# Performance work log

Hardware: AMD Instinct MI355X
Metric: run time of the kernel (lower is better)

Reference implementation:

```python
import jax, jax.numpy as jnp
import numpy as np

N = 100000   # nodes
E = 1000000  # edges per block
P = 100000   # pos/neg link edges
IN = 128
H = 64


def setup_inputs() -> dict:
    key = jax.random.key(0)
    ks = jax.random.split(key, 24)
    d = {}
    d["x"] = jax.random.normal(ks[0], (N, IN), jnp.float32)
    d["edge_weight"] = jax.random.uniform(ks[1], (3, E), jnp.float32)
    d["src"] = jax.random.randint(ks[2], (E,), 0, N)
    d["dst"] = jax.random.randint(ks[3], (E,), 0, N)
    d["pos_src"] = jax.random.randint(ks[4], (P,), 0, N)
    d["pos_dst"] = jax.random.randint(ks[5], (P,), 0, N)
    d["neg_src"] = jax.random.randint(ks[6], (P,), 0, N)
    d["neg_dst"] = jax.random.randint(ks[7], (P,), 0, N)
    s = 1.0 / np.sqrt(IN)
    h = 1.0 / np.sqrt(H)
    d["W0"] = jax.random.normal(ks[8], (IN, H), jnp.float32) * s
    d["b0"] = jnp.zeros((H,), jnp.float32)
    d["W1"] = jax.random.normal(ks[9], (H, H), jnp.float32) * h
    d["b1"] = jnp.zeros((H,), jnp.float32)
    d["W2"] = jax.random.normal(ks[10], (H, H), jnp.float32) * h
    d["b2"] = jnp.zeros((H,), jnp.float32)
    d["P0"] = jax.random.normal(ks[11], (H, H), jnp.float32) * h
    d["pb0"] = jnp.zeros((H,), jnp.float32)
    d["P1"] = jax.random.normal(ks[12], (H, H), jnp.float32) * h
    d["pb1"] = jnp.zeros((H,), jnp.float32)
    d["P2"] = jax.random.normal(ks[13], (H, 1), jnp.float32) * h
    d["pb2"] = jnp.zeros((1,), jnp.float32)
    return d


def _graph_conv(h, W, b, src, dst, ew, n_nodes):
    # DGL GraphConv, norm='both': D_out^{-1/2} on source feats,
    # edge-weighted sum aggregation, D_in^{-1/2} on result, then linear.
    ones = jnp.ones(src.shape[0], h.dtype)
    deg_out = jax.ops.segment_sum(ones, src, num_segments=n_nodes)
    deg_in = jax.ops.segment_sum(ones, dst, num_segments=n_nodes)
    norm_src = jax.lax.rsqrt(jnp.maximum(deg_out, 1.0))
    norm_dst = jax.lax.rsqrt(jnp.maximum(deg_in, 1.0))
    # apply weight before aggregation (in_feats >= out_feats); math-equivalent either way
    hw = (h * norm_src[:, None]) @ W            # [N, H]
    msg = hw[src] * ew[:, None]                 # [E, H] gather + scale
    agg = jax.ops.segment_sum(msg, dst, num_segments=n_nodes)  # scatter-add
    return agg * norm_dst[:, None] + b


def reference(x, edge_weight, src, dst, pos_src, pos_dst, neg_src, neg_dst,
              W0, b0, W1, b1, W2, b2, P0, pb0, P1, pb1, P2, pb2):
    h = jax.nn.relu(_graph_conv(x, W0, b0, src, dst, edge_weight[0], N))
    h = jax.nn.relu(_graph_conv(h, W1, b1, src, dst, edge_weight[1], N))
    h = _graph_conv(h, W2, b2, src, dst, edge_weight[2], N)  # no relu on last layer

    def mlp(z):
        z = jax.nn.relu(z @ P0 + pb0)
        z = jax.nn.relu(z @ P1 + pb1)
        return z @ P2 + pb2

    h_pos = mlp(h[pos_src] * h[pos_dst])  # [P, 1]
    h_neg = mlp(h[neg_src] * h[neg_dst])  # [P, 1]
    return (h_pos, h_neg)
```

## Files before the change

kernel.cpp:

```cpp
#include <hip/hip_runtime.h>


#define NN 100000
#define NE 1000000
#define NP 100000
#define SCAN_NB 98

__device__ __forceinline__ void row_fma(float4& acc, float xv, const float4& wv) {
    acc.x = fmaf(xv, wv.x, acc.x);
    acc.y = fmaf(xv, wv.y, acc.y);
    acc.z = fmaf(xv, wv.z, acc.z);
    acc.w = fmaf(xv, wv.w, acc.w);
}

__global__ void deg_kernel(const int4* __restrict__ src4, const int4* __restrict__ dst4,
                           int* __restrict__ repl, int E4) {
    int xcc;
    asm volatile("s_getreg_b32 %0, hwreg(HW_REG_XCC_ID)" : "=s"(xcc));
    xcc &= 7;
    int* dout = repl + xcc * NN;
    int* din  = repl + (8 + xcc) * NN;
    int tid = blockIdx.x * blockDim.x + threadIdx.x;
    if (tid < E4) {
        int4 s = src4[tid], d = dst4[tid];
        __hip_atomic_fetch_add(&dout[s.x], 1, __ATOMIC_RELAXED, __HIP_MEMORY_SCOPE_WORKGROUP);
        __hip_atomic_fetch_add(&dout[s.y], 1, __ATOMIC_RELAXED, __HIP_MEMORY_SCOPE_WORKGROUP);
        __hip_atomic_fetch_add(&dout[s.z], 1, __ATOMIC_RELAXED, __HIP_MEMORY_SCOPE_WORKGROUP);
        __hip_atomic_fetch_add(&dout[s.w], 1, __ATOMIC_RELAXED, __HIP_MEMORY_SCOPE_WORKGROUP);
        __hip_atomic_fetch_add(&din[d.x], 1, __ATOMIC_RELAXED, __HIP_MEMORY_SCOPE_WORKGROUP);
        __hip_atomic_fetch_add(&din[d.y], 1, __ATOMIC_RELAXED, __HIP_MEMORY_SCOPE_WORKGROUP);
        __hip_atomic_fetch_add(&din[d.z], 1, __ATOMIC_RELAXED, __HIP_MEMORY_SCOPE_WORKGROUP);
        __hip_atomic_fetch_add(&din[d.w], 1, __ATOMIC_RELAXED, __HIP_MEMORY_SCOPE_WORKGROUP);
    }
}

__global__ void reduce_norm_kernel(const int* __restrict__ repl, float* __restrict__ norm_src,
                                   float* __restrict__ norm_dst, int* __restrict__ deg_in, int n) {
    int i = blockIdx.x * blockDim.x + threadIdx.x;
    if (i < n) {
        int so = 0, si = 0;
#pragma unroll
        for (int x = 0; x < 8; ++x) {
            so += repl[x * NN + i];
            si += repl[(8 + x) * NN + i];
        }
        norm_src[i] = rsqrtf(fmaxf((float)so, 1.0f));
        norm_dst[i] = rsqrtf(fmaxf((float)si, 1.0f));
        deg_in[i] = si;
    }
}

__global__ __launch_bounds__(1024) void scan_block(const int* __restrict__ deg,
                                                   int* __restrict__ tmp_excl,
                                                   int* __restrict__ blocksums, int n) {
    __shared__ int wsums[16];
    const int i = blockIdx.x * 1024 + threadIdx.x;
    const int lane = threadIdx.x & 63, w = threadIdx.x >> 6;
    int v = (i < n) ? deg[i] : 0;
    int s = v;
#pragma unroll
    for (int off = 1; off < 64; off <<= 1) {
        int u = __shfl_up(s, off, 64);
        if (lane >= off) s += u;
    }
    if (lane == 63) wsums[w] = s;
    __syncthreads();
    if (w == 0) {
        int wv = (lane < 16) ? wsums[lane] : 0;
#pragma unroll
        for (int off = 1; off < 16; off <<= 1) {
            int u = __shfl_up(wv, off, 64);
            if (lane >= off) wv += u;
        }
        if (lane < 16) wsums[lane] = wv;
    }
    __syncthreads();
    int excl = s - v + (w > 0 ? wsums[w - 1] : 0);
    if (i < n) tmp_excl[i] = excl;
    if (threadIdx.x == 1023) blocksums[blockIdx.x] = excl + v;
}

__global__ void scan_sums(int* __restrict__ bs, int nb) {
    __shared__ int wtot[2];
    const int t = threadIdx.x;
    const int lane = t & 63, w = t >> 6;
    int v = (t < nb) ? bs[t] : 0;
    int s = v;
#pragma unroll
    for (int off = 1; off < 64; off <<= 1) {
        int u = __shfl_up(s, off, 64);
        if (lane >= off) s += u;
    }
    if (lane == 63) wtot[w] = s;
    __syncthreads();
    int excl = s - v + (w == 1 ? wtot[0] : 0);
    if (t < nb) bs[t] = excl;
}

__global__ __launch_bounds__(1024) void scan_apply(const int* __restrict__ tmp_excl,
                                                   const int* __restrict__ bs,
                                                   int* __restrict__ row_ptr,
                                                   int* __restrict__ cursor, int n) {
    const int i = blockIdx.x * 1024 + threadIdx.x;
    if (i < n) {
        int r = tmp_excl[i] + bs[blockIdx.x];
        row_ptr[i] = r;
        cursor[i] = r;
    }
    if (i == 0) row_ptr[n] = NE;
}

__global__ void csr_fill(const int* __restrict__ src, const int* __restrict__ dst,
                         const float* __restrict__ ew, int* __restrict__ cursor,
                         float4* __restrict__ cedge, int E) {
    int tid = blockIdx.x * blockDim.x + threadIdx.x;
    int stride = gridDim.x * blockDim.x;
    for (int e = tid; e < E; e += stride) {
        int d = dst[e];
        int slot = atomicAdd(&cursor[d], 1);
        float4 c;
        c.x = __int_as_float(src[e]);
        c.y = ew[e];
        c.z = ew[NE + e];
        c.w = ew[2 * NE + e];
        cedge[slot] = c;
    }
}

template <int WSEL, bool FINAL>
__global__ __launch_bounds__(256) void aggregate(const float* __restrict__ hw,
                                                 const float4* __restrict__ cedge,
                                                 const int* __restrict__ row_ptr,
                                                 const float* __restrict__ norm_src,
                                                 const float* __restrict__ norm_dst,
                                                 const float* __restrict__ bias,
                                                 float* __restrict__ outx, int n) {
    const int lane = threadIdx.x & 63;
    const int gw = (blockIdx.x * blockDim.x + threadIdx.x) >> 6;
    const int nw = (gridDim.x * blockDim.x) >> 6;
    const float blane = bias[lane];
    for (int node = gw; node < n; node += nw) {
        int beg = row_ptr[node], end = row_ptr[node + 1];
        float a0 = 0.f, a1 = 0.f, a2 = 0.f, a3 = 0.f;
        int i = beg;
        for (; i + 7 < end; i += 8) {
            float4 c0 = cedge[i + 0], c1 = cedge[i + 1], c2 = cedge[i + 2], c3 = cedge[i + 3];
            float4 c4 = cedge[i + 4], c5 = cedge[i + 5], c6 = cedge[i + 6], c7 = cedge[i + 7];
            float h0 = hw[__float_as_int(c0.x) * 64 + lane];
            float h1 = hw[__float_as_int(c1.x) * 64 + lane];
            float h2 = hw[__float_as_int(c2.x) * 64 + lane];
            float h3 = hw[__float_as_int(c3.x) * 64 + lane];
            float h4 = hw[__float_as_int(c4.x) * 64 + lane];
            float h5 = hw[__float_as_int(c5.x) * 64 + lane];
            float h6 = hw[__float_as_int(c6.x) * 64 + lane];
            float h7 = hw[__float_as_int(c7.x) * 64 + lane];
            a0 = fmaf(h0, (WSEL == 0) ? c0.y : (WSEL == 1) ? c0.z : c0.w, a0);
            a1 = fmaf(h1, (WSEL == 0) ? c1.y : (WSEL == 1) ? c1.z : c1.w, a1);
            a2 = fmaf(h2, (WSEL == 0) ? c2.y : (WSEL == 1) ? c2.z : c2.w, a2);
            a3 = fmaf(h3, (WSEL == 0) ? c3.y : (WSEL == 1) ? c3.z : c3.w, a3);
            a0 = fmaf(h4, (WSEL == 0) ? c4.y : (WSEL == 1) ? c4.z : c4.w, a0);
            a1 = fmaf(h5, (WSEL == 0) ? c5.y : (WSEL == 1) ? c5.z : c5.w, a1);
            a2 = fmaf(h6, (WSEL == 0) ? c6.y : (WSEL == 1) ? c6.z : c6.w, a2);
            a3 = fmaf(h7, (WSEL == 0) ? c7.y : (WSEL == 1) ? c7.z : c7.w, a3);
        }
        for (; i + 1 < end; i += 2) {
            float4 c0 = cedge[i], c1 = cedge[i + 1];
            float h0 = hw[__float_as_int(c0.x) * 64 + lane];
            float h1 = hw[__float_as_int(c1.x) * 64 + lane];
            a0 = fmaf(h0, (WSEL == 0) ? c0.y : (WSEL == 1) ? c0.z : c0.w, a0);
            a1 = fmaf(h1, (WSEL == 0) ? c1.y : (WSEL == 1) ? c1.z : c1.w, a1);
        }
        if (i < end) {
            float4 c0 = cedge[i];
            float h0 = hw[__float_as_int(c0.x) * 64 + lane];
            a0 = fmaf(h0, (WSEL == 0) ? c0.y : (WSEL == 1) ? c0.z : c0.w, a0);
        }
        float a = (a0 + a1) + (a2 + a3);
        float nd = norm_dst[node];
        float t;
        if (FINAL) {
            t = fmaf(a, nd, blane);
        } else {
            t = fmaxf(fmaf(a, nd, blane), 0.f) * norm_src[node];
        }
        outx[node * 64 + lane] = t;
    }
}

template <int K, bool SCALE>
__global__ __launch_bounds__(256, 5) void gemm_tile(const float* __restrict__ in,
                                                    const float* __restrict__ W,
                                                    const float* __restrict__ norm_src,
                                                    float* __restrict__ out, int n) {
    __shared__ float Ws[K * 64];
    const int tid = threadIdx.x;
    for (int i = tid; i < K * 16; i += 256) ((float4*)Ws)[i] = ((const float4*)W)[i];
    __syncthreads();

    const int tr = tid >> 4, tc = tid & 15;
    const int row0 = blockIdx.x * 64 + tr * 4;
    const float* xr0 = in + (size_t)min(row0 + 0, n - 1) * K;
    const float* xr1 = in + (size_t)min(row0 + 1, n - 1) * K;
    const float* xr2 = in + (size_t)min(row0 + 2, n - 1) * K;
    const float* xr3 = in + (size_t)min(row0 + 3, n - 1) * K;

    float4 acc0 = {0, 0, 0, 0}, acc1 = {0, 0, 0, 0}, acc2 = {0, 0, 0, 0}, acc3 = {0, 0, 0, 0};
#pragma unroll 4
    for (int k4 = 0; k4 < K / 4; ++k4) {
        const int kb = k4 * 4;
        float4 xv0 = *(const float4*)&xr0[kb];
        float4 xv1 = *(const float4*)&xr1[kb];
        float4 xv2 = *(const float4*)&xr2[kb];
        float4 xv3 = *(const float4*)&xr3[kb];
        const float* wb = &Ws[kb * 64 + tc * 4];
        float4 wk;
        wk = *(const float4*)(wb);
        row_fma(acc0, xv0.x, wk); row_fma(acc1, xv1.x, wk); row_fma(acc2, xv2.x, wk); row_fma(acc3, xv3.x, wk);
        wk = *(const float4*)(wb + 64);
        row_fma(acc0, xv0.y, wk); row_fma(acc1, xv1.y, wk); row_fma(acc2, xv2.y, wk); row_fma(acc3, xv3.y, wk);
        wk = *(const float4*)(wb + 128);
        row_fma(acc0, xv0.z, wk); row_fma(acc1, xv1.z, wk); row_fma(acc2, xv2.z, wk); row_fma(acc3, xv3.z, wk);
        wk = *(const float4*)(wb + 192);
        row_fma(acc0, xv0.w, wk); row_fma(acc1, xv1.w, wk); row_fma(acc2, xv2.w, wk); row_fma(acc3, xv3.w, wk);
    }

#pragma unroll
    for (int i = 0; i < 4; ++i) {
        int row = row0 + i;
        if (row < n) {
            float4 o = (i == 0) ? acc0 : (i == 1) ? acc1 : (i == 2) ? acc2 : acc3;
            if (SCALE) {
                float ns = norm_src[row];
                o.x *= ns; o.y *= ns; o.z *= ns; o.w *= ns;
            }
            *(float4*)&out[row * 64 + tc * 4] = o;
        }
    }
}

#define ZST 76

__global__ __launch_bounds__(256) void mlp_tile(const float* __restrict__ hfin,
                                                const float* __restrict__ P0,
                                                const float* __restrict__ pb0,
                                                const float* __restrict__ P1,
                                                const float* __restrict__ pb1,
                                                const float* __restrict__ P2,
                                                const float* __restrict__ pb2,
                                                const int* __restrict__ pos_src,
                                                const int* __restrict__ pos_dst,
                                                const int* __restrict__ neg_src,
                                                const int* __restrict__ neg_dst,
                                                float* __restrict__ out, int P) {
    __shared__ float Zs[64][ZST];
    __shared__ float pb0s[64], pb1s[64], P2s[64];
    __shared__ int pas[64], pbs[64];
    const int tid = threadIdx.x;
    const int base = blockIdx.x << 6;
    if (tid < 64) {
        pb0s[tid] = pb0[tid];
        pb1s[tid] = pb1[tid];
        P2s[tid] = P2[tid];
        int p = base + tid;
        pas[tid] = (p < P) ? pos_src[p] : neg_src[p - P];
        pbs[tid] = (p < P) ? pos_dst[p] : neg_dst[p - P];
    }
    const float pb2v = pb2[0];
    const int lane = tid & 63, w = tid >> 6;
    const int tr = tid >> 4, tc = tid & 15;
    __syncthreads();

    {
        const int pbase = w * 16;
#pragma unroll
        for (int r = 0; r < 2; ++r) {
            const int p0 = pbase + r * 8;
            int a0 = pas[p0 + 0], b0 = pbs[p0 + 0];
            int a1 = pas[p0 + 1], b1 = pbs[p0 + 1];
            int a2 = pas[p0 + 2], b2 = pbs[p0 + 2];
            int a3 = pas[p0 + 3], b3 = pbs[p0 + 3];
            int a4 = pas[p0 + 4], b4 = pbs[p0 + 4];
            int a5 = pas[p0 + 5], b5 = pbs[p0 + 5];
            int a6 = pas[p0 + 6], b6 = pbs[p0 + 6];
            int a7 = pas[p0 + 7], b7 = pbs[p0 + 7];
            float ha0 = hfin[a0 * 64 + lane], hb0 = hfin[b0 * 64 + lane];
            float ha1 = hfin[a1 * 64 + lane], hb1 = hfin[b1 * 64 + lane];
            float ha2 = hfin[a2 * 64 + lane], hb2 = hfin[b2 * 64 + lane];
            float ha3 = hfin[a3 * 64 + lane], hb3 = hfin[b3 * 64 + lane];
            float ha4 = hfin[a4 * 64 + lane], hb4 = hfin[b4 * 64 + lane];
            float ha5 = hfin[a5 * 64 + lane], hb5 = hfin[b5 * 64 + lane];
            float ha6 = hfin[a6 * 64 + lane], hb6 = hfin[b6 * 64 + lane];
            float ha7 = hfin[a7 * 64 + lane], hb7 = hfin[b7 * 64 + lane];
            Zs[p0 + 0][lane] = ha0 * hb0;
            Zs[p0 + 1][lane] = ha1 * hb1;
            Zs[p0 + 2][lane] = ha2 * hb2;
            Zs[p0 + 3][lane] = ha3 * hb3;
            Zs[p0 + 4][lane] = ha4 * hb4;
            Zs[p0 + 5][lane] = ha5 * hb5;
            Zs[p0 + 6][lane] = ha6 * hb6;
            Zs[p0 + 7][lane] = ha7 * hb7;
        }
    }
    __syncthreads();

    float4 acc0, acc1, acc2, acc3;
    {
        float4 binit = *(const float4*)&pb0s[tc * 4];
        acc0 = binit; acc1 = binit; acc2 = binit; acc3 = binit;
    }
#pragma unroll 4
    for (int k4 = 0; k4 < 16; ++k4) {
        const int kb = k4 * 4;
        float4 xv0 = *(const float4*)&Zs[tr * 4 + 0][kb];
        float4 xv1 = *(const float4*)&Zs[tr * 4 + 1][kb];
        float4 xv2 = *(const float4*)&Zs[tr * 4 + 2][kb];
        float4 xv3 = *(const float4*)&Zs[tr * 4 + 3][kb];
        const float* wb = &P0[kb * 64 + tc * 4];
        float4 wk;
        wk = *(const float4*)(wb);
        row_fma(acc0, xv0.x, wk); row_fma(acc1, xv1.x, wk); row_fma(acc2, xv2.x, wk); row_fma(acc3, xv3.x, wk);
        wk = *(const float4*)(wb + 64);
        row_fma(acc0, xv0.y, wk); row_fma(acc1, xv1.y, wk); row_fma(acc2, xv2.y, wk); row_fma(acc3, xv3.y, wk);
        wk = *(const float4*)(wb + 128);
        row_fma(acc0, xv0.z, wk); row_fma(acc1, xv1.z, wk); row_fma(acc2, xv2.z, wk); row_fma(acc3, xv3.z, wk);
        wk = *(const float4*)(wb + 192);
        row_fma(acc0, xv0.w, wk); row_fma(acc1, xv1.w, wk); row_fma(acc2, xv2.w, wk); row_fma(acc3, xv3.w, wk);
    }
    __syncthreads();
#pragma unroll
    for (int i = 0; i < 4; ++i) {
        float4 o = (i == 0) ? acc0 : (i == 1) ? acc1 : (i == 2) ? acc2 : acc3;
        o.x = fmaxf(o.x, 0.f); o.y = fmaxf(o.y, 0.f); o.z = fmaxf(o.z, 0.f); o.w = fmaxf(o.w, 0.f);
        *(float4*)&Zs[tr * 4 + i][tc * 4] = o;
    }
    __syncthreads();

    {
        float4 binit = *(const float4*)&pb1s[tc * 4];
        acc0 = binit; acc1 = binit; acc2 = binit; acc3 = binit;
    }
#pragma unroll 4
    for (int k4 = 0; k4 < 16; ++k4) {
        const int kb = k4 * 4;
        float4 xv0 = *(const float4*)&Zs[tr * 4 + 0][kb];
        float4 xv1 = *(const float4*)&Zs[tr * 4 + 1][kb];
        float4 xv2 = *(const float4*)&Zs[tr * 4 + 2][kb];
        float4 xv3 = *(const float4*)&Zs[tr * 4 + 3][kb];
        const float* wb = &P1[kb * 64 + tc * 4];
        float4 wk;
        wk = *(const float4*)(wb);
        row_fma(acc0, xv0.x, wk); row_fma(acc1, xv1.x, wk); row_fma(acc2, xv2.x, wk); row_fma(acc3, xv3.x, wk);
        wk = *(const float4*)(wb + 64);
        row_fma(acc0, xv0.y, wk); row_fma(acc1, xv1.y, wk); row_fma(acc2, xv2.y, wk); row_fma(acc3, xv3.y, wk);
        wk = *(const float4*)(wb + 128);
        row_fma(acc0, xv0.z, wk); row_fma(acc1, xv1.z, wk); row_fma(acc2, xv2.z, wk); row_fma(acc3, xv3.z, wk);
        wk = *(const float4*)(wb + 192);
        row_fma(acc0, xv0.w, wk); row_fma(acc1, xv1.w, wk); row_fma(acc2, xv2.w, wk); row_fma(acc3, xv3.w, wk);
    }
    __syncthreads();
#pragma unroll
    for (int i = 0; i < 4; ++i) {
        float4 o = (i == 0) ? acc0 : (i == 1) ? acc1 : (i == 2) ? acc2 : acc3;
        o.x = fmaxf(o.x, 0.f); o.y = fmaxf(o.y, 0.f); o.z = fmaxf(o.z, 0.f); o.w = fmaxf(o.w, 0.f);
        *(float4*)&Zs[tr * 4 + i][tc * 4] = o;
    }
    __syncthreads();

    {
        int p = tid >> 2, kq = tid & 3;
        float s = 0.f;
#pragma unroll
        for (int i = 0; i < 16; ++i) s = fmaf(Zs[p][kq * 16 + i], P2s[kq * 16 + i], s);
        s += __shfl_xor(s, 1, 64);
        s += __shfl_xor(s, 2, 64);
        if (kq == 0) out[base + p] = s + pb2v;
    }
}

extern "C" void kernel_launch(void* const* d_in, const int* in_sizes, int n_in,
                              void* d_out, int out_size, void* d_ws, size_t ws_size,
                              hipStream_t stream) {
    const float* x     = (const float*)d_in[0];
    const float* ew    = (const float*)d_in[1];
    const int* src     = (const int*)d_in[2];
    const int* dst     = (const int*)d_in[3];
    const int* pos_src = (const int*)d_in[4];
    const int* pos_dst = (const int*)d_in[5];
    const int* neg_src = (const int*)d_in[6];
    const int* neg_dst = (const int*)d_in[7];
    const float* W0    = (const float*)d_in[8];
    const float* b0    = (const float*)d_in[9];
    const float* W1    = (const float*)d_in[10];
    const float* b1    = (const float*)d_in[11];
    const float* W2    = (const float*)d_in[12];
    const float* b2    = (const float*)d_in[13];
    const float* P0    = (const float*)d_in[14];
    const float* pb0   = (const float*)d_in[15];
    const float* P1    = (const float*)d_in[16];
    const float* pb1   = (const float*)d_in[17];
    const float* P2    = (const float*)d_in[18];
    const float* pb2   = (const float*)d_in[19];
    float* out = (float*)d_out;

    float* ws = (float*)d_ws;
    float* norm_src = ws;
    float* norm_dst = ws + 100000;
    int* cursor     = (int*)(ws + 200000);
    int* deg_in     = (int*)(ws + 300000);
    int* row_ptr    = (int*)(ws + 400000);
    float4* cedge   = (float4*)(ws + 500004);
    float* hw       = ws + 4500004;
    float* agg      = ws + 10900004;

    int* repl      = (int*)hw;
    int* tmp_excl  = (int*)hw + 16 * NN;
    int* blocksums = (int*)hw + 17 * NN;

    hipMemsetAsync(repl, 0, 16 * NN * sizeof(int), stream);
    deg_kernel<<<(NE / 4 + 255) / 256, 256, 0, stream>>>((const int4*)src, (const int4*)dst,
                                                         repl, NE / 4);
    reduce_norm_kernel<<<(NN + 255) / 256, 256, 0, stream>>>(repl, norm_src, norm_dst, deg_in, NN);
    scan_block<<<SCAN_NB, 1024, 0, stream>>>(deg_in, tmp_excl, blocksums, NN);
    scan_sums<<<1, 128, 0, stream>>>(blocksums, SCAN_NB);
    scan_apply<<<SCAN_NB, 1024, 0, stream>>>(tmp_excl, blocksums, row_ptr, cursor, NN);
    csr_fill<<<2048, 256, 0, stream>>>(src, dst, ew, cursor, cedge, NE);

    const int NT = (NN + 63) / 64;

    gemm_tile<128, true><<<NT, 256, 0, stream>>>(x, W0, norm_src, hw, NN);
    aggregate<0, false><<<4096, 256, 0, stream>>>(hw, cedge, row_ptr, norm_src, norm_dst, b0, agg, NN);
    gemm_tile<64, false><<<NT, 256, 0, stream>>>(agg, W1, nullptr, hw, NN);
    aggregate<1, false><<<4096, 256, 0, stream>>>(hw, cedge, row_ptr, norm_src, norm_dst, b1, agg, NN);
    gemm_tile<64, false><<<NT, 256, 0, stream>>>(agg, W2, nullptr, hw, NN);
    aggregate<2, true><<<4096, 256, 0, stream>>>(hw, cedge, row_ptr, norm_src, norm_dst, b2, agg, NN);

    mlp_tile<<<(2 * NP) / 64, 256, 0, stream>>>(agg, P0, pb0, P1, pb1, P2, pb2,
                                                pos_src, pos_dst, neg_src, neg_dst, out, NP);
}
```

Before: 489.0 us.

## Fuse aggregation and dense transform per layer, fold source norm into edge weights

Each GraphConv layer now gathers and aggregates input features first, then applies the weight matrix inside the same kernel. Each wave handles 4 nodes, stages their aggregated rows in LDS and multiplies by W held in shared memory. The separate gemm_tile launches and the intermediate hw/agg round trips through global memory go away. norm_src is folded into the per-edge weights in csr_fill, so no row scaling is needed. The trade-off is that layer 0 now gathers 128-wide x rows per edge instead of 64-wide transformed rows, which doubles that layer's gather traffic.

Measured after the change: 480.0 us. Within noise of the previous version (-1.8%).

```diff
diff --git a/kernel.cpp b/kernel.cpp
--- a/kernel.cpp
+++ b/kernel.cpp
@@ -111,130 +111,131 @@
 }
 
 __global__ void csr_fill(const int* __restrict__ src, const int* __restrict__ dst,
-                         const float* __restrict__ ew, int* __restrict__ cursor,
-                         float4* __restrict__ cedge, int E) {
+                         const float* __restrict__ ew, const float* __restrict__ norm_src,
+                         int* __restrict__ cursor, float4* __restrict__ cedge, int E) {
     int tid = blockIdx.x * blockDim.x + threadIdx.x;
     int stride = gridDim.x * blockDim.x;
     for (int e = tid; e < E; e += stride) {
+        int s = src[e];
         int d = dst[e];
+        float nsv = norm_src[s];
         int slot = atomicAdd(&cursor[d], 1);
         float4 c;
-        c.x = __int_as_float(src[e]);
-        c.y = ew[e];
-        c.z = ew[NE + e];
-        c.w = ew[2 * NE + e];
+        c.x = __int_as_float(s);
+        c.y = ew[e] * nsv;
+        c.z = ew[NE + e] * nsv;
+        c.w = ew[2 * NE + e] * nsv;
         cedge[slot] = c;
     }
 }
 
-template <int WSEL, bool FINAL>
-__global__ __launch_bounds__(256) void aggregate(const float* __restrict__ hw,
-                                                 const float4* __restrict__ cedge,
-                                                 const int* __restrict__ row_ptr,
-                                                 const float* __restrict__ norm_src,
-                                                 const float* __restrict__ norm_dst,
-                                                 const float* __restrict__ bias,
-                                                 float* __restrict__ outx, int n) {
-    const int lane = threadIdx.x & 63;
-    const int gw = (blockIdx.x * blockDim.x + threadIdx.x) >> 6;
-    const int nw = (gridDim.x * blockDim.x) >> 6;
-    const float blane = bias[lane];
-    for (int node = gw; node < n; node += nw) {
-        int beg = row_ptr[node], end = row_ptr[node + 1];
-        float a0 = 0.f, a1 = 0.f, a2 = 0.f, a3 = 0.f;
-        int i = beg;
-        for (; i + 7 < end; i += 8) {
-            float4 c0 = cedge[i + 0], c1 = cedge[i + 1], c2 = cedge[i + 2], c3 = cedge[i + 3];
-            float4 c4 = cedge[i + 4], c5 = cedge[i + 5], c6 = cedge[i + 6], c7 = cedge[i + 7];
-            float h0 = hw[__float_as_int(c0.x) * 64 + lane];
-            float h1 = hw[__float_as_int(c1.x) * 64 + lane];
-            float h2 = hw[__float_as_int(c2.x) * 64 + lane];
-            float h3 = hw[__float_as_int(c3.x) * 64 + lane];
-            float h4 = hw[__float_as_int(c4.x) * 64 + lane];
-            float h5 = hw[__float_as_int(c5.x) * 64 + lane];
-            float h6 = hw[__float_as_int(c6.x) * 64 + lane];
-            float h7 = hw[__float_as_int(c7.x) * 64 + lane];
-            a0 = fmaf(h0, (WSEL == 0) ? c0.y : (WSEL == 1) ? c0.z : c0.w, a0);
-            a1 = fmaf(h1, (WSEL == 0) ? c1.y : (WSEL == 1) ? c1.z : c1.w, a1);
-            a2 = fmaf(h2, (WSEL == 0) ? c2.y : (WSEL == 1) ? c2.z : c2.w, a2);
-            a3 = fmaf(h3, (WSEL == 0) ? c3.y : (WSEL == 1) ? c3.z : c3.w, a3);
-            a0 = fmaf(h4, (WSEL == 0) ? c4.y : (WSEL == 1) ? c4.z : c4.w, a0);
-            a1 = fmaf(h5, (WSEL == 0) ? c5.y : (WSEL == 1) ? c5.z : c5.w, a1);
-            a2 = fmaf(h6, (WSEL == 0) ? c6.y : (WSEL == 1) ? c6.z : c6.w, a2);
-            a3 = fmaf(h7, (WSEL == 0) ? c7.y : (WSEL == 1) ? c7.z : c7.w, a3);
-        }
-        for (; i + 1 < end; i += 2) {
-            float4 c0 = cedge[i], c1 = cedge[i + 1];
-            float h0 = hw[__float_as_int(c0.x) * 64 + lane];
-            float h1 = hw[__float_as_int(c1.x) * 64 + lane];
-            a0 = fmaf(h0, (WSEL == 0) ? c0.y : (WSEL == 1) ? c0.z : c0.w, a0);
-            a1 = fmaf(h1, (WSEL == 0) ? c1.y : (WSEL == 1) ? c1.z : c1.w, a1);
-        }
-        if (i < end) {
-            float4 c0 = cedge[i];
-            float h0 = hw[__float_as_int(c0.x) * 64 + lane];
-            a0 = fmaf(h0, (WSEL == 0) ? c0.y : (WSEL == 1) ? c0.z : c0.w, a0);
-        }
-        float a = (a0 + a1) + (a2 + a3);
-        float nd = norm_dst[node];
-        float t;
-        if (FINAL) {
-            t = fmaf(a, nd, blane);
-        } else {
-            t = fmaxf(fmaf(a, nd, blane), 0.f) * norm_src[node];
-        }
-        outx[node * 64 + lane] = t;
-    }
-}
-
-template <int K, bool SCALE>
-__global__ __launch_bounds__(256, 5) void gemm_tile(const float* __restrict__ in,
-                                                    const float* __restrict__ W,
-                                                    const float* __restrict__ norm_src,
-                                                    float* __restrict__ out, int n) {
+template <int K, int WSEL, bool FINAL>
+__global__ __launch_bounds__(256) void fused_layer(const float* __restrict__ tin,
+                                                   const float4* __restrict__ cedge,
+                                                   const int* __restrict__ row_ptr,
+                                                   const float* __restrict__ W,
+                                                   const float* __restrict__ bias,
+                                                   const float* __restrict__ norm_dst,
+                                                   float* __restrict__ tout, int n4) {
     __shared__ float Ws[K * 64];
+    __shared__ float At[4][K * 4];
     const int tid = threadIdx.x;
     for (int i = tid; i < K * 16; i += 256) ((float4*)Ws)[i] = ((const float4*)W)[i];
     __syncthreads();
 
-    const int tr = tid >> 4, tc = tid & 15;
-    const int row0 = blockIdx.x * 64 + tr * 4;
-    const float* xr0 = in + (size_t)min(row0 + 0, n - 1) * K;
-    const float* xr1 = in + (size_t)min(row0 + 1, n - 1) * K;
-    const float* xr2 = in + (size_t)min(row0 + 2, n - 1) * K;
-    const float* xr3 = in + (size_t)min(row0 + 3, n - 1) * K;
-
-    float4 acc0 = {0, 0, 0, 0}, acc1 = {0, 0, 0, 0}, acc2 = {0, 0, 0, 0}, acc3 = {0, 0, 0, 0};
-#pragma unroll 4
-    for (int k4 = 0; k4 < K / 4; ++k4) {
-        const int kb = k4 * 4;
-        float4 xv0 = *(const float4*)&xr0[kb];
-        float4 xv1 = *(const float4*)&xr1[kb];
-        float4 xv2 = *(const float4*)&xr2[kb];
-        float4 xv3 = *(const float4*)&xr3[kb];
-        const float* wb = &Ws[kb * 64 + tc * 4];
-        float4 wk;
-        wk = *(const float4*)(wb);
-        row_fma(acc0, xv0.x, wk); row_fma(acc1, xv1.x, wk); row_fma(acc2, xv2.x, wk); row_fma(acc3, xv3.x, wk);
-        wk = *(const float4*)(wb + 64);
-        row_fma(acc0, xv0.y, wk); row_fma(acc1, xv1.y, wk); row_fma(acc2, xv2.y, wk); row_fma(acc3, xv3.y, wk);
-        wk = *(const float4*)(wb + 128);
-        row_fma(acc0, xv0.z, wk); row_fma(acc1, xv1.z, wk); row_fma(acc2, xv2.z, wk); row_fma(acc3, xv3.z, wk);
-        wk = *(const float4*)(wb + 192);
-        row_fma(acc0, xv0.w, wk); row_fma(acc1, xv1.w, wk); row_fma(acc2, xv2.w, wk); row_fma(acc3, xv3.w, wk);
-    }
-
-#pragma unroll
-    for (int i = 0; i < 4; ++i) {
-        int row = row0 + i;
-        if (row < n) {
-            float4 o = (i == 0) ? acc0 : (i == 1) ? acc1 : (i == 2) ? acc2 : acc3;
-            if (SCALE) {
-                float ns = norm_src[row];
-                o.x *= ns; o.y *= ns; o.z *= ns; o.w *= ns;
+    const int lane = tid & 63, wv = tid >> 6;
+    const int gw = (blockIdx.x * 256 + tid) >> 6;
+    const int nw = (gridDim.x * 256) >> 6;
+    const float blane = bias[lane];
+    float* at = &At[wv][0];
+
+    for (int g = gw; g < n4; g += nw) {
+        const int node0 = g * 4;
+#pragma unroll
+        for (int j = 0; j < 4; ++j) {
+            const int node = node0 + j;
+            const int beg = row_ptr[node], end = row_ptr[node + 1];
+            if (K == 64) {
+                float a0 = 0.f, a1 = 0.f, a2 = 0.f, a3 = 0.f;
+                int i = beg;
+                for (; i + 7 < end; i += 8) {
+                    float4 c0 = cedge[i + 0], c1 = cedge[i + 1], c2 = cedge[i + 2], c3 = cedge[i + 3];
+                    float4 c4 = cedge[i + 4], c5 = cedge[i + 5], c6 = cedge[i + 6], c7 = cedge[i + 7];
+                    float h0 = tin[__float_as_int(c0.x) * 64 + lane];
+                    float h1 = tin[__float_as_int(c1.x) * 64 + lane];
+                    float h2 = tin[__float_as_int(c2.x) * 64 + lane];
+                    float h3 = tin[__float_as_int(c3.x) * 64 + lane];
+                    float h4 = tin[__float_as_int(c4.x) * 64 + lane];
+                    float h5 = tin[__float_as_int(c5.x) * 64 + lane];
+                    float h6 = tin[__float_as_int(c6.x) * 64 + lane];
+                    float h7 = tin[__float_as_int(c7.x) * 64 + lane];
+                    a0 = fmaf(h0, (WSEL == 0) ? c0.y : (WSEL == 1) ? c0.z : c0.w, a0);
+                    a1 = fmaf(h1, (WSEL == 0) ? c1.y : (WSEL == 1) ? c1.z : c1.w, a1);
+                    a2 = fmaf(h2, (WSEL == 0) ? c2.y : (WSEL == 1) ? c2.z : c2.w, a2);
+                    a3 = fmaf(h3, (WSEL == 0) ? c3.y : (WSEL == 1) ? c3.z : c3.w, a3);
+                    a0 = fmaf(h4, (WSEL == 0) ? c4.y : (WSEL == 1) ? c4.z : c4.w, a0);
+                    a1 = fmaf(h5, (WSEL == 0) ? c5.y : (WSEL == 1) ? c5.z : c5.w, a1);
+                    a2 = fmaf(h6, (WSEL == 0) ? c6.y : (WSEL == 1) ? c6.z : c6.w, a2);
+                    a3 = fmaf(h7, (WSEL == 0) ? c7.y : (WSEL == 1) ? c7.z : c7.w, a3);
+                }
+                for (; i < end; ++i) {
+                    float4 c0 = cedge[i];
+                    float h0 = tin[__float_as_int(c0.x) * 64 + lane];
+                    a0 = fmaf(h0, (WSEL == 0) ? c0.y : (WSEL == 1) ? c0.z : c0.w, a0);
+                }
+                at[lane * 4 + j] = (a0 + a1) + (a2 + a3);
+            } else {
+                float l0a = 0.f, l1a = 0.f, h0a = 0.f, h1a = 0.f;
+                int i = beg;
+                for (; i + 3 < end; i += 4) {
+                    float4 c0 = cedge[i + 0], c1 = cedge[i + 1], c2 = cedge[i + 2], c3 = cedge[i + 3];
+                    int s0 = __float_as_int(c0.x), s1 = __float_as_int(c1.x);
+                    int s2 = __float_as_int(c2.x), s3 = __float_as_int(c3.x);
+                    float lo0 = tin[s0 * 128 + lane], hi0 = tin[s0 * 128 + 64 + lane];
+                    float lo1 = tin[s1 * 128 + lane], hi1 = tin[s1 * 128 + 64 + lane];
+                    float lo2 = tin[s2 * 128 + lane], hi2 = tin[s2 * 128 + 64 + lane];
+                    float lo3 = tin[s3 * 128 + lane], hi3 = tin[s3 * 128 + 64 + lane];
+                    float w0 = (WSEL == 0) ? c0.y : (WSEL == 1) ? c0.z : c0.w;
+                    float w1 = (WSEL == 0) ? c1.y : (WSEL == 1) ? c1.z : c1.w;
+                    float w2 = (WSEL == 0) ? c2.y : (WSEL == 1) ? c2.z : c2.w;
+                    float w3 = (WSEL == 0) ? c3.y : (WSEL == 1) ? c3.z : c3.w;
+                    l0a = fmaf(lo0, w0, l0a); h0a = fmaf(hi0, w0, h0a);
+                    l1a = fmaf(lo1, w1, l1a); h1a = fmaf(hi1, w1, h1a);
+                    l0a = fmaf(lo2, w2, l0a); h0a = fmaf(hi2, w2, h0a);
+                    l1a = fmaf(lo3, w3, l1a); h1a = fmaf(hi3, w3, h1a);
+                }
+                for (; i < end; ++i) {
+                    float4 c0 = cedge[i];
+                    int s0 = __float_as_int(c0.x);
+                    float w0 = (WSEL == 0) ? c0.y : (WSEL == 1) ? c0.z : c0.w;
+                    l0a = fmaf(tin[s0 * 128 + lane], w0, l0a);
+                    h0a = fmaf(tin[s0 * 128 + 64 + lane], w0, h0a);
+                }
+                at[lane * 4 + j] = l0a + l1a;
+                at[(64 + lane) * 4 + j] = h0a + h1a;
             }
-            *(float4*)&out[row * 64 + tc * 4] = o;
-        }
+        }
+        asm volatile("s_waitcnt lgkmcnt(0)" ::: "memory");
+
+        float acc0 = 0.f, acc1 = 0.f, acc2 = 0.f, acc3 = 0.f;
+#pragma unroll 8
+        for (int k = 0; k < K; ++k) {
+            float4 av = *(const float4*)&at[k * 4];
+            float wval = Ws[k * 64 + lane];
+            acc0 = fmaf(av.x, wval, acc0);
+            acc1 = fmaf(av.y, wval, acc1);
+            acc2 = fmaf(av.z, wval, acc2);
+            acc3 = fmaf(av.w, wval, acc3);
+        }
+#pragma unroll
+        for (int j = 0; j < 4; ++j) {
+            float acc = (j == 0) ? acc0 : (j == 1) ? acc1 : (j == 2) ? acc2 : acc3;
+            float nd = norm_dst[node0 + j];
+            float t = fmaf(acc, nd, blane);
+            if (!FINAL) t = fmaxf(t, 0.f);
+            tout[(node0 + j) * 64 + lane] = t;
+        }
+        asm volatile("s_waitcnt lgkmcnt(0)" ::: "memory");
     }
 }
 
@@ -409,12 +410,12 @@
     int* deg_in     = (int*)(ws + 300000);
     int* row_ptr    = (int*)(ws + 400000);
     float4* cedge   = (float4*)(ws + 500004);
-    float* hw       = ws + 4500004;
-    float* agg      = ws + 10900004;
-
-    int* repl      = (int*)hw;
-    int* tmp_excl  = (int*)hw + 16 * NN;
-    int* blocksums = (int*)hw + 17 * NN;
+    float* tA       = ws + 4500004;
+    float* tB       = ws + 10900004;
+
+    int* repl      = (int*)tA;
+    int* tmp_excl  = (int*)tA + 16 * NN;
+    int* blocksums = (int*)tA + 17 * NN;
 
     hipMemsetAsync(repl, 0, 16 * NN * sizeof(int), stream);
     deg_kernel<<<(NE / 4 + 255) / 256, 256, 0, stream>>>((const int4*)src, (const int4*)dst,
@@ -423,17 +424,14 @@
     scan_block<<<SCAN_NB, 1024, 0, stream>>>(deg_in, tmp_excl, blocksums, NN);
     scan_sums<<<1, 128, 0, stream>>>(blocksums, SCAN_NB);
     scan_apply<<<SCAN_NB, 1024, 0, stream>>>(tmp_excl, blocksums, row_ptr, cursor, NN);
-    csr_fill<<<2048, 256, 0, stream>>>(src, dst, ew, cursor, cedge, NE);
-
-    const int NT = (NN + 63) / 64;
-
-    gemm_tile<128, true><<<NT, 256, 0, stream>>>(x, W0, norm_src, hw, NN);
-    aggregate<0, false><<<4096, 256, 0, stream>>>(hw, cedge, row_ptr, norm_src, norm_dst, b0, agg, NN);
-    gemm_tile<64, false><<<NT, 256, 0, stream>>>(agg, W1, nullptr, hw, NN);
-    aggregate<1, false><<<4096, 256, 0, stream>>>(hw, cedge, row_ptr, norm_src, norm_dst, b1, agg, NN);
-    gemm_tile<64, false><<<NT, 256, 0, stream>>>(agg, W2, nullptr, hw, NN);
-    aggregate<2, true><<<4096, 256, 0, stream>>>(hw, cedge, row_ptr, norm_src, norm_dst, b2, agg, NN);
-
-    mlp_tile<<<(2 * NP) / 64, 256, 0, stream>>>(agg, P0, pb0, P1, pb1, P2, pb2,
+    csr_fill<<<2048, 256, 0, stream>>>(src, dst, ew, norm_src, cursor, cedge, NE);
+
+    const int NG = NN / 4;
+
+    fused_layer<128, 0, false><<<4096, 256, 0, stream>>>(x, cedge, row_ptr, W0, b0, norm_dst, tA, NG);
+    fused_layer<64, 1, false><<<4096, 256, 0, stream>>>(tA, cedge, row_ptr, W1, b1, norm_dst, tB, NG);
+    fused_layer<64, 2, true><<<4096, 256, 0, stream>>>(tB, cedge, row_ptr, W2, b2, norm_dst, tA, NG);
+
+    mlp_tile<<<(2 * NP) / 64, 256, 0, stream>>>(tA, P0, pb0, P1, pb1, P2, pb2,
                                                 pos_src, pos_dst, neg_src, neg_dst, out, NP);
 }
```

## Fold source-degree norm into CSR edge weights and prefetch GEMM input rows

Applied to the files above, without the earlier changes.

The D_out^{-1/2} source normalisation is now multiplied into the per-edge weights once, during CSR construction. This removes the per-node norm_src scaling from the GEMM epilogue and from the aggregate epilogue across all three layers. The gemm_tile loop is fully unrolled and software-pipelined, loading the next float4 of each input row while computing the current one. The launch_bounds occupancy hint of 5 is dropped, which may raise register use. csr_fill now does an extra random gather of norm_src per edge.

Result: slower. 1.135 ms (+132.2%).

```diff
diff --git a/kernel.cpp b/kernel.cpp
--- a/kernel.cpp
+++ b/kernel.cpp
@@ -111,27 +111,28 @@
 }
 
 __global__ void csr_fill(const int* __restrict__ src, const int* __restrict__ dst,
-                         const float* __restrict__ ew, int* __restrict__ cursor,
-                         float4* __restrict__ cedge, int E) {
+                         const float* __restrict__ ew, const float* __restrict__ norm_src,
+                         int* __restrict__ cursor, float4* __restrict__ cedge, int E) {
     int tid = blockIdx.x * blockDim.x + threadIdx.x;
     int stride = gridDim.x * blockDim.x;
     for (int e = tid; e < E; e += stride) {
+        int s = src[e];
         int d = dst[e];
+        float nsv = norm_src[s];
         int slot = atomicAdd(&cursor[d], 1);
         float4 c;
-        c.x = __int_as_float(src[e]);
-        c.y = ew[e];
-        c.z = ew[NE + e];
-        c.w = ew[2 * NE + e];
+        c.x = __int_as_float(s);
+        c.y = ew[e] * nsv;
+        c.z = ew[NE + e] * nsv;
+        c.w = ew[2 * NE + e] * nsv;
         cedge[slot] = c;
     }
 }
 
-template <int WSEL, bool FINAL>
+template <int WSEL, bool RELU>
 __global__ __launch_bounds__(256) void aggregate(const float* __restrict__ hw,
                                                  const float4* __restrict__ cedge,
                                                  const int* __restrict__ row_ptr,
-                                                 const float* __restrict__ norm_src,
                                                  const float* __restrict__ norm_dst,
                                                  const float* __restrict__ bias,
                                                  float* __restrict__ outx, int n) {
@@ -176,22 +177,16 @@
             a0 = fmaf(h0, (WSEL == 0) ? c0.y : (WSEL == 1) ? c0.z : c0.w, a0);
         }
         float a = (a0 + a1) + (a2 + a3);
-        float nd = norm_dst[node];
-        float t;
-        if (FINAL) {
-            t = fmaf(a, nd, blane);
-        } else {
-            t = fmaxf(fmaf(a, nd, blane), 0.f) * norm_src[node];
-        }
+        float t = fmaf(a, norm_dst[node], blane);
+        if (RELU) t = fmaxf(t, 0.f);
         outx[node * 64 + lane] = t;
     }
 }
 
-template <int K, bool SCALE>
-__global__ __launch_bounds__(256, 5) void gemm_tile(const float* __restrict__ in,
-                                                    const float* __restrict__ W,
-                                                    const float* __restrict__ norm_src,
-                                                    float* __restrict__ out, int n) {
+template <int K>
+__global__ __launch_bounds__(256) void gemm_tile(const float* __restrict__ in,
+                                                 const float* __restrict__ W,
+                                                 float* __restrict__ out, int n) {
     __shared__ float Ws[K * 64];
     const int tid = threadIdx.x;
     for (int i = tid; i < K * 16; i += 256) ((float4*)Ws)[i] = ((const float4*)W)[i];
@@ -205,23 +200,32 @@
     const float* xr3 = in + (size_t)min(row0 + 3, n - 1) * K;
 
     float4 acc0 = {0, 0, 0, 0}, acc1 = {0, 0, 0, 0}, acc2 = {0, 0, 0, 0}, acc3 = {0, 0, 0, 0};
-#pragma unroll 4
+    float4 cur0 = *(const float4*)&xr0[0];
+    float4 cur1 = *(const float4*)&xr1[0];
+    float4 cur2 = *(const float4*)&xr2[0];
+    float4 cur3 = *(const float4*)&xr3[0];
+#pragma unroll
     for (int k4 = 0; k4 < K / 4; ++k4) {
+        float4 nxt0, nxt1, nxt2, nxt3;
+        if (k4 + 1 < K / 4) {
+            const int kb = (k4 + 1) * 4;
+            nxt0 = *(const float4*)&xr0[kb];
+            nxt1 = *(const float4*)&xr1[kb];
+            nxt2 = *(const float4*)&xr2[kb];
+            nxt3 = *(const float4*)&xr3[kb];
+        }
         const int kb = k4 * 4;
-        float4 xv0 = *(const float4*)&xr0[kb];
-        float4 xv1 = *(const float4*)&xr1[kb];
-        float4 xv2 = *(const float4*)&xr2[kb];
-        float4 xv3 = *(const float4*)&xr3[kb];
         const float* wb = &Ws[kb * 64 + tc * 4];
         float4 wk;
         wk = *(const float4*)(wb);
-        row_fma(acc0, xv0.x, wk); row_fma(acc1, xv1.x, wk); row_fma(acc2, xv2.x, wk); row_fma(acc3, xv3.x, wk);
+        row_fma(acc0, cur0.x, wk); row_fma(acc1, cur1.x, wk); row_fma(acc2, cur2.x, wk); row_fma(acc3, cur3.x, wk);
         wk = *(const float4*)(wb + 64);
-        row_fma(acc0, xv0.y, wk); row_fma(acc1, xv1.y, wk); row_fma(acc2, xv2.y, wk); row_fma(acc3, xv3.y, wk);
+        row_fma(acc0, cur0.y, wk); row_fma(acc1, cur1.y, wk); row_fma(acc2, cur2.y, wk); row_fma(acc3, cur3.y, wk);
         wk = *(const float4*)(wb + 128);
-        row_fma(acc0, xv0.z, wk); row_fma(acc1, xv1.z, wk); row_fma(acc2, xv2.z, wk); row_fma(acc3, xv3.z, wk);
+        row_fma(acc0, cur0.z, wk); row_fma(acc1, cur1.z, wk); row_fma(acc2, cur2.z, wk); row_fma(acc3, cur3.z, wk);
         wk = *(const float4*)(wb + 192);
-        row_fma(acc0, xv0.w, wk); row_fma(acc1, xv1.w, wk); row_fma(acc2, xv2.w, wk); row_fma(acc3, xv3.w, wk);
+        row_fma(acc0, cur0.w, wk); row_fma(acc1, cur1.w, wk); row_fma(acc2, cur2.w, wk); row_fma(acc3, cur3.w, wk);
+        cur0 = nxt0; cur1 = nxt1; cur2 = nxt2; cur3 = nxt3;
     }
 
 #pragma unroll
@@ -229,10 +233,6 @@
         int row = row0 + i;
         if (row < n) {
             float4 o = (i == 0) ? acc0 : (i == 1) ? acc1 : (i == 2) ? acc2 : acc3;
-            if (SCALE) {
-                float ns = norm_src[row];
-                o.x *= ns; o.y *= ns; o.z *= ns; o.w *= ns;
-            }
             *(float4*)&out[row * 64 + tc * 4] = o;
         }
     }
@@ -423,16 +423,16 @@
     scan_block<<<SCAN_NB, 1024, 0, stream>>>(deg_in, tmp_excl, blocksums, NN);
     scan_sums<<<1, 128, 0, stream>>>(blocksums, SCAN_NB);
     scan_apply<<<SCAN_NB, 1024, 0, stream>>>(tmp_excl, blocksums, row_ptr, cursor, NN);
-    csr_fill<<<2048, 256, 0, stream>>>(src, dst, ew, cursor, cedge, NE);
+    csr_fill<<<2048, 256, 0, stream>>>(src, dst, ew, norm_src, cursor, cedge, NE);
 
     const int NT = (NN + 63) / 64;
 
-    gemm_tile<128, true><<<NT, 256, 0, stream>>>(x, W0, norm_src, hw, NN);
-    aggregate<0, false><<<4096, 256, 0, stream>>>(hw, cedge, row_ptr, norm_src, norm_dst, b0, agg, NN);
-    gemm_tile<64, false><<<NT, 256, 0, stream>>>(agg, W1, nullptr, hw, NN);
-    aggregate<1, false><<<4096, 256, 0, stream>>>(hw, cedge, row_ptr, norm_src, norm_dst, b1, agg, NN);
-    gemm_tile<64, false><<<NT, 256, 0, stream>>>(agg, W2, nullptr, hw, NN);
-    aggregate<2, true><<<4096, 256, 0, stream>>>(hw, cedge, row_ptr, norm_src, norm_dst, b2, agg, NN);
+    gemm_tile<128><<<NT, 256, 0, stream>>>(x, W0, hw, NN);
+    aggregate<0, true><<<4096, 256, 0, stream>>>(hw, cedge, row_ptr, norm_dst, b0, agg, NN);
+    gemm_tile<64><<<NT, 256, 0, stream>>>(agg, W1, hw, NN);
+    aggregate<1, true><<<4096, 256, 0, stream>>>(hw, cedge, row_ptr, norm_dst, b1, agg, NN);
+    gemm_tile<64><<<NT, 256, 0, stream>>>(agg, W2, hw, NN);
+    aggregate<2, false><<<4096, 256, 0, stream>>>(hw, cedge, row_ptr, norm_dst, b2, agg, NN);
 
     mlp_tile<<<(2 * NP) / 64, 256, 0, stream>>>(agg, P0, pb0, P1, pb1, P2, pb2,
                                                 pos_src, pos_dst, neg_src, neg_dst, out, NP);
```
